# Kernel tuning notes

Measured on AMD Instinct MI355X. Metric: run time of the kernel, lower is better.

Reference implementation:

```python
import jax, jax.numpy as jnp
import numpy as np

KERNELS = (4, 4, 8, 8, 8, 16, 16)
HEADS = (4, 4, 8, 8, 8, 16, 16)
PATCH = 2
EPS = 1e-5


def _layer_norm(x, w, b):
    mu = jnp.mean(x, axis=-1, keepdims=True)
    var = jnp.mean(jnp.square(x - mu), axis=-1, keepdims=True)
    return (x - mu) * jax.lax.rsqrt(var + EPS) * w + b


def _sliding_kernel_attention(x, w_qkv, k, heads):
    # x: (B, H, W, C) channels-last. Unfold -> per-window attention over the
    # k*k pixels (token dim = C) -> overlap-add fold (stride 1).
    B, H, W, C = x.shape
    Lh, Lw = H - k + 1, W - k + 1
    scale = (C // heads) ** -0.5
    ih = jnp.arange(Lh)[:, None] + jnp.arange(k)[None, :]   # (Lh, k)
    iw = jnp.arange(Lw)[:, None] + jnp.arange(k)[None, :]   # (Lw, k)
    pat = x[:, ih][:, :, :, iw]                             # (B, Lh, k, Lw, k, C)
    tok = pat.transpose(0, 1, 3, 2, 4, 5).reshape(B, Lh * Lw, k * k, C)
    qkv = jnp.einsum('blnc,dc->blnd', tok, w_qkv)           # (B, L, k*k, 3C)
    q, kk, v = jnp.split(qkv, 3, axis=-1)
    attn = jax.nn.softmax(jnp.einsum('blqc,blkc->blqk', q, kk) * scale, axis=-1)
    o = jnp.einsum('blqk,blkc->blqc', attn, v)              # (B, L, k*k, C)
    o = o.reshape(B, Lh, Lw, k, k, C).transpose(0, 1, 3, 2, 4, 5)  # (B,Lh,k,Lw,k,C)
    # overlap-add fold back to (B, H, W, C); duplicate indices accumulate
    return jnp.zeros_like(x).at[:, ih[:, :, None, None], iw[None, None, :, :], :].add(o)


def _block(x, ln1_w, ln1_b, w_qkv, ln2_w, ln2_b, w1, b1, w2, b2, k, heads):
    x = x + _sliding_kernel_attention(_layer_norm(x, ln1_w, ln1_b), w_qkv, k, heads)
    h = _layer_norm(x, ln2_w, ln2_b)
    h = jax.nn.gelu(h @ w1.T + b1, approximate=False)
    return x + (h @ w2.T + b2)


def _forward(x, patch_w, patch_b, row_emb, col_emb, cls_tok, ln1_w, ln1_b, qkv_w,
             ln2_w, ln2_b, mlp_w1, mlp_b1, mlp_w2, mlp_b2, cls_w, cls_b):
    # patch embed: conv k=stride=PATCH; output laid out channels-last (B, G, G, C)
    h = jax.lax.conv_general_dilated(
        x, patch_w, (PATCH, PATCH), 'VALID',
        dimension_numbers=('NCHW', 'OIHW', 'NHWC')) + patch_b
    B, G, _, C = h.shape
    # 2D positional embedding: row half + col half concatenated on channels
    pos = jnp.concatenate([
        jnp.broadcast_to(row_emb[:, None, :], (G, G, C // 2)),
        jnp.broadcast_to(col_emb[None, :, :], (G, G, C // 2))], axis=-1)
    h = h + pos
    # cls token: one extra row prepended along H (torch cat on dim=2)
    cls = jnp.broadcast_to(cls_tok, (B, 1, G, C))
    h = jnp.concatenate([cls, h], axis=1)                   # (B, G+1, G, C)
    for i in range(7):
        h = _block(h, ln1_w[i], ln1_b[i], qkv_w[i], ln2_w[i], ln2_b[i],
                   mlp_w1[i], mlp_b1[i], mlp_w2[i], mlp_b2[i],
                   KERNELS[i], HEADS[i])
    return h[:, 0, 0, :] @ cls_w.T + cls_b                  # (B, num_classes)


def setup_inputs() -> dict:
    key = jax.random.key(0)
    ks = jax.random.split(key, 8)
    B, C, G, NCLS, NB = 16, 256, 16, 1000, 7
    s = 0.02
    return {
        'x': jax.random.normal(ks[0], (B, 3, 32, 32), jnp.float32),
        'patch_w': jax.random.normal(ks[1], (C, 3, PATCH, PATCH), jnp.float32) * s,
        'patch_b': jnp.zeros((C,), jnp.float32),
        'row_emb': jax.random.normal(ks[2], (G, C // 2), jnp.float32) * s,
        'col_emb': jax.random.normal(ks[3], (G, C // 2), jnp.float32) * s,
        'cls_tok': jnp.zeros((C,), jnp.float32),
        'ln1_w': jnp.ones((NB, C), jnp.float32),
        'ln1_b': jnp.zeros((NB, C), jnp.float32),
        'qkv_w': jax.random.normal(ks[4], (NB, 3 * C, C), jnp.float32) * s,
        'ln2_w': jnp.ones((NB, C), jnp.float32),
        'ln2_b': jnp.zeros((NB, C), jnp.float32),
        'mlp_w1': jax.random.normal(ks[5], (NB, 2 * C, C), jnp.float32) * s,
        'mlp_b1': jnp.zeros((NB, 2 * C), jnp.float32),
        'mlp_w2': jax.random.normal(ks[6], (NB, C, 2 * C), jnp.float32) * s,
        'mlp_b2': jnp.zeros((NB, C), jnp.float32),
        'cls_w': jax.random.normal(ks[7], (NCLS, C), jnp.float32) * s,
        'cls_b': jnp.zeros((NCLS,), jnp.float32),
    }


def reference(x, patch_w, patch_b, row_emb, col_emb, cls_tok, ln1_w, ln1_b, qkv_w,
              ln2_w, ln2_b, mlp_w1, mlp_b1, mlp_w2, mlp_b2, cls_w, cls_b):
    return _forward(x, patch_w, patch_b, row_emb, col_emb, cls_tok, ln1_w, ln1_b,
                    qkv_w, ln2_w, ln2_b, mlp_w1, mlp_b1, mlp_w2, mlp_b2, cls_w, cls_b)
```

## Files before the change

kernel.cpp:

```cpp
#include <hip/hip_runtime.h>
#include <cmath>

#define NPIX 4352
#define C_DIM 256

typedef unsigned short ushort_t;
typedef unsigned int uint_t;
typedef float f32x4 __attribute__((ext_vector_type(4)));
typedef __bf16 bfx8 __attribute__((ext_vector_type(8)));

__device__ __forceinline__ ushort_t f2bf(float f) {
    uint_t u = __float_as_uint(f);
    u = (u + 0x7FFFu + ((u >> 16) & 1u)) >> 16;
    return (ushort_t)u;
}
__device__ __forceinline__ float bf2f(ushort_t b) {
    return __uint_as_float(((uint_t)b) << 16);
}
__device__ __forceinline__ float gelu_f(float v) {
    return 0.5f * v * (1.0f + erff(v * 0.70710678118654752f));
}

__global__ __launch_bounds__(256) void conv3_bf16(
    const float* __restrict__ a, ushort_t* __restrict__ oa, int na,
    const float* __restrict__ b, ushort_t* __restrict__ ob, int nb,
    const float* __restrict__ c, ushort_t* __restrict__ oc, int nc)
{
    int ntot = na + nb + nc;
    for (int i = blockIdx.x * 256 + threadIdx.x; i < ntot; i += gridDim.x * 256) {
        if (i < na)            oa[i] = f2bf(a[i]);
        else if (i < na + nb)  ob[i - na] = f2bf(b[i - na]);
        else                   oc[i - na - nb] = f2bf(c[i - na - nb]);
    }
}

__global__ __launch_bounds__(256) void patch_embed_ln(
    const float* __restrict__ x, const float* __restrict__ pw,
    const float* __restrict__ pb, const float* __restrict__ row_emb,
    const float* __restrict__ col_emb, const float* __restrict__ cls_tok,
    const float* __restrict__ lw, const float* __restrict__ lb,
    float* __restrict__ out, ushort_t* __restrict__ lnout)
{
    __shared__ float red[8];
    int p = blockIdx.x;
    int c = threadIdx.x;
    int b = p / 272;
    int rem = p - b * 272;
    int y = rem >> 4;
    int xw = rem & 15;
    float v;
    if (y == 0) {
        v = cls_tok[c];
    } else {
        int gr = y - 1, gc = xw;
        const float* xb = x + (size_t)b * 3 * 1024;
        const float* wc = pw + (size_t)c * 12;
        float acc = pb[c];
        #pragma unroll
        for (int ci = 0; ci < 3; ci++)
            #pragma unroll
            for (int ph = 0; ph < 2; ph++)
                #pragma unroll
                for (int pq = 0; pq < 2; pq++)
                    acc += xb[ci * 1024 + (2 * gr + ph) * 32 + (2 * gc + pq)]
                         * wc[(ci * 2 + ph) * 2 + pq];
        acc += (c < 128) ? row_emb[gr * 128 + c] : col_emb[gc * 128 + (c - 128)];
        v = acc;
    }
    out[(size_t)p * C_DIM + c] = v;
    float s = v;
    s += __shfl_down(s, 32); s += __shfl_down(s, 16); s += __shfl_down(s, 8);
    s += __shfl_down(s, 4);  s += __shfl_down(s, 2);  s += __shfl_down(s, 1);
    if ((c & 63) == 0) red[c >> 6] = s;
    __syncthreads();
    float mu = (red[0] + red[1] + red[2] + red[3]) * (1.0f / 256.0f);
    float d = v - mu;
    float s2 = d * d;
    s2 += __shfl_down(s2, 32); s2 += __shfl_down(s2, 16); s2 += __shfl_down(s2, 8);
    s2 += __shfl_down(s2, 4);  s2 += __shfl_down(s2, 2);  s2 += __shfl_down(s2, 1);
    if ((c & 63) == 0) red[4 + (c >> 6)] = s2;
    __syncthreads();
    float var = (red[4] + red[5] + red[6] + red[7]) * (1.0f / 256.0f);
    lnout[(size_t)p * C_DIM + c] = f2bf(d * rsqrtf(var + 1e-5f) * lw[c] + lb[c]);
}

__global__ __launch_bounds__(256) void layernorm_k(
    const float* __restrict__ in, const float* __restrict__ w,
    const float* __restrict__ b, ushort_t* __restrict__ out)
{
    __shared__ float red[8];
    int r = blockIdx.x, c = threadIdx.x;
    float v = in[(size_t)r * C_DIM + c];
    float s = v;
    s += __shfl_down(s, 32); s += __shfl_down(s, 16); s += __shfl_down(s, 8);
    s += __shfl_down(s, 4);  s += __shfl_down(s, 2);  s += __shfl_down(s, 1);
    if ((c & 63) == 0) red[c >> 6] = s;
    __syncthreads();
    float mu = (red[0] + red[1] + red[2] + red[3]) * (1.0f / 256.0f);
    float d = v - mu;
    float s2 = d * d;
    s2 += __shfl_down(s2, 32); s2 += __shfl_down(s2, 16); s2 += __shfl_down(s2, 8);
    s2 += __shfl_down(s2, 4);  s2 += __shfl_down(s2, 2);  s2 += __shfl_down(s2, 1);
    if ((c & 63) == 0) red[4 + (c >> 6)] = s2;
    __syncthreads();
    float var = (red[4] + red[5] + red[6] + red[7]) * (1.0f / 256.0f);
    out[(size_t)r * C_DIM + c] = f2bf(d * rsqrtf(var + 1e-5f) * w[c] + b[c]);
}

template <int BM, int BN, int MODE>
__global__ __launch_bounds__(256) void gemm_v2(
    const ushort_t* __restrict__ A, const ushort_t* __restrict__ B,
    const float* __restrict__ bias, const float* __restrict__ res,
    void* __restrict__ outp, ushort_t* __restrict__ vT, int K, int ldo)
{
    constexpr int MI = BM / 32, NJ = BN / 32;
    constexpr int AG = BM * 4, BG = BN * 4;
    constexpr int AU = AG / 256, BU = BG / 256;
    constexpr int HALF = (BM + BN) * 32;
    constexpr int STAGE_E = 2 * HALF;
    constexpr int BOUNCE_E = BM * (BN + 8);
    constexpr int SMEM_E = (STAGE_E > BOUNCE_E) ? STAGE_E : BOUNCE_E;
    __shared__ ushort_t sm[SMEM_E];

    int m0 = blockIdx.x * BM, n0 = blockIdx.y * BN;
    int t = threadIdx.x, lane = t & 63, wv = t >> 6;
    int l15 = lane & 15, lg = lane >> 4;
    int wr = wv >> 1, wc = wv & 1;

    const int nt = K / 32;
    f32x4 acc[MI][NJ] = {};
    uint4 ra[AU], rb[BU];

    #pragma unroll
    for (int u = 0; u < AU; u++) {
        int g = t + u * 256, row = g >> 2, p = g & 3;
        int ps = p ^ ((row >> 1) & 3);
        ra[u] = *(const uint4*)(A + (size_t)(m0 + row) * K + ps * 8);
    }
    #pragma unroll
    for (int u = 0; u < BU; u++) {
        int g = t + u * 256, col = g >> 2, p = g & 3;
        int ps = p ^ ((col >> 1) & 3);
        rb[u] = *(const uint4*)(B + (size_t)(n0 + col) * K + ps * 8);
    }
    #pragma unroll
    for (int u = 0; u < AU; u++) *(uint4*)(sm + (t + u * 256) * 8) = ra[u];
    #pragma unroll
    for (int u = 0; u < BU; u++) *(uint4*)(sm + BM * 32 + (t + u * 256) * 8) = rb[u];
    __syncthreads();

    for (int ks = 0; ks < nt; ks++) {
        int coff = (ks & 1) * HALF, noff = ((ks & 1) ^ 1) * HALF;
        if (ks + 1 < nt) {
            int k1 = (ks + 1) * 32;
            #pragma unroll
            for (int u = 0; u < AU; u++) {
                int g = t + u * 256, row = g >> 2, p = g & 3;
                int ps = p ^ ((row >> 1) & 3);
                ra[u] = *(const uint4*)(A + (size_t)(m0 + row) * K + k1 + ps * 8);
            }
            #pragma unroll
            for (int u = 0; u < BU; u++) {
                int g = t + u * 256, col = g >> 2, p = g & 3;
                int ps = p ^ ((col >> 1) & 3);
                rb[u] = *(const uint4*)(B + (size_t)(n0 + col) * K + k1 + ps * 8);
            }
        }
        bfx8 af[MI], bf[NJ];
        #pragma unroll
        for (int i = 0; i < MI; i++) {
            int row = wr * (BM / 2) + i * 16 + l15;
            af[i] = *(const bfx8*)(sm + coff + row * 32 + ((lg ^ ((row >> 1) & 3)) << 3));
        }
        #pragma unroll
        for (int j = 0; j < NJ; j++) {
            int col = wc * (BN / 2) + j * 16 + l15;
            bf[j] = *(const bfx8*)(sm + coff + BM * 32 + col * 32 + ((lg ^ ((col >> 1) & 3)) << 3));
        }
        #pragma unroll
        for (int i = 0; i < MI; i++)
            #pragma unroll
            for (int j = 0; j < NJ; j++)
                acc[i][j] = __builtin_amdgcn_mfma_f32_16x16x32_bf16(af[i], bf[j], acc[i][j], 0, 0, 0);
        if (ks + 1 < nt) {
            #pragma unroll
            for (int u = 0; u < AU; u++) *(uint4*)(sm + noff + (t + u * 256) * 8) = ra[u];
            #pragma unroll
            for (int u = 0; u < BU; u++) *(uint4*)(sm + noff + BM * 32 + (t + u * 256) * 8) = rb[u];
        }
        __syncthreads();
    }

    if (MODE == 0 && n0 >= 512) {
        #pragma unroll
        for (int i = 0; i < MI; i++) {
            int mb = m0 + wr * (BM / 2) + i * 16 + lg * 4;
            #pragma unroll
            for (int j = 0; j < NJ; j++) {
                int nv = n0 - 512 + wc * (BN / 2) + j * 16 + l15;
                ushort4 pk;
                pk.x = f2bf(acc[i][j][0]); pk.y = f2bf(acc[i][j][1]);
                pk.z = f2bf(acc[i][j][2]); pk.w = f2bf(acc[i][j][3]);
                *(ushort4*)&vT[(size_t)nv * NPIX + mb] = pk;
            }
        }
        return;
    }
    if (MODE == 3) {
        float* o = (float*)outp;
        #pragma unroll
        for (int i = 0; i < MI; i++) {
            #pragma unroll
            for (int j = 0; j < NJ; j++) {
                int col = n0 + wc * (BN / 2) + j * 16 + l15;
                float bz = bias[col];
                #pragma unroll
                for (int r = 0; r < 4; r++) {
                    int row = m0 + wr * (BM / 2) + i * 16 + lg * 4 + r;
                    o[(size_t)row * ldo + col] = acc[i][j][r] + bz + res[(size_t)row * ldo + col];
                }
            }
        }
        return;
    }
    __syncthreads();
    #pragma unroll
    for (int i = 0; i < MI; i++) {
        #pragma unroll
        for (int j = 0; j < NJ; j++) {
            int cl = wc * (BN / 2) + j * 16 + l15;
            float bz = (MODE == 2) ? bias[n0 + cl] : 0.0f;
            #pragma unroll
            for (int r = 0; r < 4; r++) {
                int rl = wr * (BM / 2) + i * 16 + lg * 4 + r;
                float v = acc[i][j][r];
                if (MODE == 2) v = gelu_f(v + bz);
                sm[rl * (BN + 8) + cl] = f2bf(v);
            }
        }
    }
    __syncthreads();
    ushort_t* ob = (ushort_t*)outp;
    #pragma unroll
    for (int e = 0; e < BM * BN; e += 2048) {
        int idx = e + t * 8;
        int rl = idx / BN, cl = idx % BN;
        uint4 v = *(const uint4*)(sm + rl * (BN + 8) + cl);
        *(uint4*)&ob[(size_t)(m0 + rl) * ldo + n0 + cl] = v;
    }
}

__device__ __forceinline__ uint2 ld_u4_align(const uint_t* drow, int e0) {
    int d0 = e0 >> 1;
    if (!(e0 & 1)) return make_uint2(drow[d0], drow[d0 + 1]);
    uint_t a = drow[d0], b = drow[d0 + 1], c = drow[d0 + 2];
    return make_uint2((a >> 16) | (b << 16), (b >> 16) | (c << 16));
}
__device__ __forceinline__ uint4 ld_u8_align(const uint_t* drow, int e0) {
    int d0 = e0 >> 1;
    if (!(e0 & 1)) return make_uint4(drow[d0], drow[d0 + 1], drow[d0 + 2], drow[d0 + 3]);
    uint_t a = drow[d0], b = drow[d0 + 1], c = drow[d0 + 2], d = drow[d0 + 3], e = drow[d0 + 4];
    return make_uint4((a >> 16) | (b << 16), (b >> 16) | (c << 16),
                      (c >> 16) | (d << 16), (d >> 16) | (e << 16));
}

template <int KK>
__global__ __launch_bounds__(256) void attn_v2(
    const ushort_t* __restrict__ qk, const ushort_t* __restrict__ vT,
    ushort_t* __restrict__ obuf, int w0, int nW, float scale)
{
    constexpr int T = KK * KK;
    constexpr int Lh = 18 - KK, Lw = 17 - KK, L = Lh * Lw;
    constexpr int NF   = 1;
    constexpr int NJ   = 8;
    constexpr int PSTR = 40;
    constexpr int KROWS = 32;
    constexpr int VROWS = 256;
    constexpr int EOFF = 2048;
    constexpr int ESTR = 128;

    __shared__ ushort_t Klds[KROWS * 256];
    __shared__ ushort_t Vlds[VROWS * 64];
    __shared__ ushort_t Plds[4][16 * PSTR];

    int t = threadIdx.x, lane = t & 63, wv = t >> 6;
    int l15 = lane & 15, lg = lane >> 4;

    int wrel = blockIdx.x * 2 + (wv & 1);
    int wloc = wv & 1, chalf = wv >> 1, qbase = 0;
    if (wrel >= nW) wrel = nW - 1;

    int pbs[2];
    #pragma unroll
    for (int w = 0; w < 2; w++) {
        int wi = blockIdx.x * 2 + w;
        if (wi >= nW) wi = nW - 1;
        wi += w0;
        int b = wi / L, lrem = wi % L;
        pbs[w] = b * 272 + (lrem / Lw) * 16 + (lrem % Lw);
    }

    int qtok = qbase + l15;
    int qpix = pbs[wloc] + ((qtok >> 2) << 4) + (qtok & 3);
    bfx8 qf[8];
    #pragma unroll
    for (int cs = 0; cs < 8; cs++)
        qf[cs] = *(const bfx8*)(qk + (size_t)qpix * 512 + cs * 32 + lg * 8);

    f32x4 o[NJ] = {};
    float lsum[4] = {0.f, 0.f, 0.f, 0.f};

    for (int g = t; g < KROWS * 32; g += 256) {
        int row = g >> 5, cg = g & 31;
        int pix = pbs[row >> 4] + (((row & 15) >> 2) << 4) + (row & 3);
        uint4 v = *(const uint4*)(qk + (size_t)pix * 512 + 256 + cg * 8);
        *(uint4*)(Klds + row * 256 + ((cg ^ (row & 7)) << 3)) = v;
    }
    for (int g = t; g < VROWS * 8; g += 256) {
        int cr = g >> 3, c16 = g & 7;
        const uint_t* drow = (const uint_t*)(vT + (size_t)cr * NPIX);
        uint4 v;
        int w = c16 >> 2, sub = c16 & 3;
        if (sub < 2) {
            int pix0 = pbs[w] + (sub << 5);
            uint2 a  = ld_u4_align(drow, pix0);
            uint2 b2 = ld_u4_align(drow, pix0 + 16);
            v = make_uint4(a.x, a.y, b2.x, b2.y);
        } else v = make_uint4(0, 0, 0, 0);
        *(uint4*)(Vlds + cr * 64 + ((c16 ^ (cr & 7)) << 3)) = v;
    }
    __syncthreads();
    f32x4 s[NF];
    #pragma unroll
    for (int j = 0; j < NF; j++) s[j] = f32x4{0.f, 0.f, 0.f, 0.f};
    #pragma unroll
    for (int cs = 0; cs < 8; cs++) {
        int krow = (wloc << 4) + l15;
        bfx8 kf = *(const bfx8*)(Klds + krow * 256 + ((((cs << 2) + lg) ^ (krow & 7)) << 3));
        s[0] = __builtin_amdgcn_mfma_f32_16x16x32_bf16(qf[cs], kf, s[0], 0, 0, 0);
    }
    float p[NF][4];
    #pragma unroll
    for (int r = 0; r < 4; r++) {
        float mx = s[0][r];
        mx = fmaxf(mx, __shfl_xor(mx, 1));
        mx = fmaxf(mx, __shfl_xor(mx, 2));
        mx = fmaxf(mx, __shfl_xor(mx, 4));
        mx = fmaxf(mx, __shfl_xor(mx, 8));
        float ps = 0.f;
        p[0][r] = __expf(scale * (s[0][r] - mx));
        ps += p[0][r];
        ps += __shfl_xor(ps, 1);
        ps += __shfl_xor(ps, 2);
        ps += __shfl_xor(ps, 4);
        ps += __shfl_xor(ps, 8);
        lsum[r] = ps;
    }
    ushort_t* Pw = Plds[wv];
    #pragma unroll
    for (int r = 0; r < 4; r++) {
        Pw[(lg * 4 + r) * PSTR + l15] = f2bf(p[0][r]);
        Pw[(lg * 4 + r) * PSTR + 16 + l15] = 0;
    }
    asm volatile("s_waitcnt lgkmcnt(0)" ::: "memory");
    __builtin_amdgcn_sched_barrier(0);
    {
        bfx8 pf = *(const bfx8*)(Pw + l15 * PSTR + (lg << 3));
        #pragma unroll
        for (int j = 0; j < NJ; j++) {
            int cr = chalf * 128 + (j << 4) + l15;
            int c16 = ((wloc << 2) + lg) ^ (cr & 7);
            bfx8 vf = *(const bfx8*)(Vlds + cr * 64 + (c16 << 3));
            o[j] = __builtin_amdgcn_mfma_f32_16x16x32_bf16(pf, vf, o[j], 0, 0, 0);
        }
    }
    asm volatile("s_waitcnt lgkmcnt(0)" ::: "memory");
    __syncthreads();
    float inv[4];
    #pragma unroll
    for (int r = 0; r < 4; r++) inv[r] = 1.0f / lsum[r];
    ushort_t* Ep = Klds + wv * EOFF;
    #pragma unroll
    for (int j = 0; j < NJ; j++)
        #pragma unroll
        for (int r = 0; r < 4; r++)
            Ep[(lg * 4 + r) * ESTR + (j << 4) + l15] = f2bf(o[j][r] * inv[r]);
    asm volatile("s_waitcnt lgkmcnt(0)" ::: "memory");
    __builtin_amdgcn_sched_barrier(0);
    size_t gb = ((size_t)wrel * T + qbase) * C_DIM + chalf * 128;
    #pragma unroll
    for (int i = 0; i < 4; i++) {
        int off = i * 512 + lane * 8;
        int row = off >> 7, col = off & 127;
        uint4 v = *(const uint4*)(Ep + row * ESTR + col);
        *(uint4*)(obuf + gb + (size_t)row * C_DIM + col) = v;
    }
}

__global__ __launch_bounds__(256) void attn_v3(
    const ushort_t* __restrict__ qk, const ushort_t* __restrict__ vT,
    ushort_t* __restrict__ obuf, int w0, float scale)
{
    __shared__ ushort_t SH[32768];
    const int Lw = 9, L = 90;
    int t = threadIdx.x, lane = t & 63, wv = t >> 6;
    int l15 = lane & 15, lg = lane >> 4;
    int wrel = blockIdx.x;
    int widx = w0 + wrel;
    int b = widx / L, lrem = widx % L;
    int pbase = b * 272 + (lrem / Lw) * 16 + (lrem % Lw);
    int qbase = wv * 16;

    int qtok = qbase + l15;
    int qpix = pbase + ((qtok >> 3) << 4) + (qtok & 7);
    bfx8 qf[8];
    #pragma unroll
    for (int cs = 0; cs < 8; cs++)
        qf[cs] = *(const bfx8*)(qk + (size_t)qpix * 512 + cs * 32 + lg * 8);

    for (int g = t; g < 64 * 32; g += 256) {
        int row = g >> 5, cg = g & 31;
        int pix = pbase + ((row >> 3) << 4) + (row & 7);
        uint4 v = *(const uint4*)(qk + (size_t)pix * 512 + 256 + cg * 8);
        *(uint4*)(SH + row * 256 + ((cg ^ (row & 7)) << 3)) = v;
    }
    for (int g = t; g < 256 * 8; g += 256) {
        int cr = g >> 3, c16 = g & 7;
        const uint_t* drow = (const uint_t*)(vT + (size_t)cr * NPIX);
        uint4 v = ld_u8_align(drow, pbase + (c16 << 4));
        *(uint4*)(SH + 16384 + cr * 64 + ((c16 ^ (cr & 7)) << 3)) = v;
    }
    __syncthreads();

    f32x4 s[4];
    #pragma unroll
    for (int j = 0; j < 4; j++) s[j] = f32x4{0.f, 0.f, 0.f, 0.f};
    #pragma unroll
    for (int cs = 0; cs < 8; cs++) {
        #pragma unroll
        for (int j = 0; j < 4; j++) {
            int krow = (j << 4) + l15;
            bfx8 kf = *(const bfx8*)(SH + krow * 256 + ((((cs << 2) + lg) ^ (krow & 7)) << 3));
            s[j] = __builtin_amdgcn_mfma_f32_16x16x32_bf16(qf[cs], kf, s[j], 0, 0, 0);
        }
    }
    float p[4][4], lsum[4];
    #pragma unroll
    for (int r = 0; r < 4; r++) {
        float mx = s[0][r];
        #pragma unroll
        for (int j = 1; j < 4; j++) mx = fmaxf(mx, s[j][r]);
        mx = fmaxf(mx, __shfl_xor(mx, 1));
        mx = fmaxf(mx, __shfl_xor(mx, 2));
        mx = fmaxf(mx, __shfl_xor(mx, 4));
        mx = fmaxf(mx, __shfl_xor(mx, 8));
        float ps = 0.f;
        #pragma unroll
        for (int j = 0; j < 4; j++) {
            p[j][r] = __expf(scale * (s[j][r] - mx));
            ps += p[j][r];
        }
        ps += __shfl_xor(ps, 1);
        ps += __shfl_xor(ps, 2);
        ps += __shfl_xor(ps, 4);
        ps += __shfl_xor(ps, 8);
        lsum[r] = ps;
    }
    __syncthreads();
    ushort_t* Pw = SH + wv * 1088;
    #pragma unroll
    for (int j = 0; j < 4; j++)
        #pragma unroll
        for (int r = 0; r < 4; r++)
            Pw[(lg * 4 + r) * 68 + (j << 4) + l15] = f2bf(p[j][r]);
    asm volatile("s_waitcnt lgkmcnt(0)" ::: "memory");
    __builtin_amdgcn_sched_barrier(0);
    f32x4 o[16] = {};
    #pragma unroll
    for (int kt = 0; kt < 2; kt++) {
        bfx8 pf = *(const bfx8*)(Pw + l15 * 68 + (kt << 5) + (lg << 3));
        #pragma unroll
        for (int j = 0; j < 16; j++) {
            int cr = (j << 4) + l15;
            int c16 = ((kt << 2) + lg) ^ (cr & 7);
            bfx8 vf = *(const bfx8*)(SH + 16384 + cr * 64 + (c16 << 3));
            o[j] = __builtin_amdgcn_mfma_f32_16x16x32_bf16(pf, vf, o[j], 0, 0, 0);
        }
    }
    asm volatile("s_waitcnt lgkmcnt(0)" ::: "memory");
    __syncthreads();
    float inv[4];
    #pragma unroll
    for (int r = 0; r < 4; r++) inv[r] = 1.0f / lsum[r];
    ushort_t* Ep = SH + wv * 4224;
    #pragma unroll
    for (int j = 0; j < 16; j++)
        #pragma unroll
        for (int r = 0; r < 4; r++)
            Ep[(lg * 4 + r) * 260 + (j << 4) + l15] = f2bf(o[j][r] * inv[r]);
    asm volatile("s_waitcnt lgkmcnt(0)" ::: "memory");
    __builtin_amdgcn_sched_barrier(0);
    size_t gb = ((size_t)wrel * 64 + qbase) * C_DIM;
    #pragma unroll
    for (int i = 0; i < 8; i++) {
        int off = i * 512 + lane * 8;
        int row = off >> 8, col = off & 255;
        uint4 v = *(const uint4*)(Ep + row * 260 + col);
        *(uint4*)(obuf + gb + off) = v;
    }
}

template <int PASS>
__global__ __launch_bounds__(256) void gemm_seq(
    const ushort_t* __restrict__ A, const ushort_t* __restrict__ B,
    const float* __restrict__ linv, void* __restrict__ outp)
{
    __shared__ ushort_t sm[8192];
    int m0 = blockIdx.x * 64, n0 = blockIdx.y * 64;
    int seq = blockIdx.z;
    int pbase = (seq >> 1) * 272 + (seq & 1) * 16;
    int t = threadIdx.x, lane = t & 63, wv = t >> 6;
    int l15 = lane & 15, lg = lane >> 4;
    int wr = wv >> 1, wc = wv & 1;

    f32x4 acc[2][2] = {};
    uint4 ra, rb;

    int g_row = t >> 2, g_p = t & 3;
    int g_ps = g_p ^ ((g_row >> 1) & 3);

    const ushort_t* Asrc;
    const ushort_t* Bsrc;
    if (PASS == 0) {
        Asrc = A + (size_t)(pbase + m0 + g_row) * 512 + g_ps * 8;
        Bsrc = B + (size_t)(pbase + n0 + g_row) * 512 + 256 + g_ps * 8;
    } else {
        Asrc = A + (size_t)seq * 65536 + (size_t)(m0 + g_row) * 256 + g_ps * 8;
        Bsrc = B + (size_t)(n0 + g_row) * NPIX + pbase + g_ps * 8;
    }

    ra = *(const uint4*)(Asrc);
    rb = *(const uint4*)(Bsrc);
    *(uint4*)(sm + t * 8) = ra;
    *(uint4*)(sm + 2048 + t * 8) = rb;
    __syncthreads();

    for (int ks = 0; ks < 8; ks++) {
        int coff = (ks & 1) * 4096, noff = ((ks & 1) ^ 1) * 4096;
        if (ks + 1 < 8) {
            int k1 = (ks + 1) * 32;
            ra = *(const uint4*)(Asrc + k1);
            rb = *(const uint4*)(Bsrc + k1);
        }
        bfx8 af[2], bf[2];
        #pragma unroll
        for (int i = 0; i < 2; i++) {
            int row = wr * 32 + i * 16 + l15;
            af[i] = *(const bfx8*)(sm + coff + row * 32 + ((lg ^ ((row >> 1) & 3)) << 3));
        }
        #pragma unroll
        for (int j = 0; j < 2; j++) {
            int col = wc * 32 + j * 16 + l15;
            bf[j] = *(const bfx8*)(sm + coff + 2048 + col * 32 + ((lg ^ ((col >> 1) & 3)) << 3));
        }
        #pragma unroll
        for (int i = 0; i < 2; i++)
            #pragma unroll
            for (int j = 0; j < 2; j++)
                acc[i][j] = __builtin_amdgcn_mfma_f32_16x16x32_bf16(af[i], bf[j], acc[i][j], 0, 0, 0);
        if (ks + 1 < 8) {
            *(uint4*)(sm + noff + t * 8) = ra;
            *(uint4*)(sm + noff + 2048 + t * 8) = rb;
        }
        __syncthreads();
    }

    if (PASS == 0) {
        float* S = (float*)outp + (size_t)seq * 65536;
        #pragma unroll
        for (int i = 0; i < 2; i++) {
            #pragma unroll
            for (int j = 0; j < 2; j++) {
                int col = n0 + wc * 32 + j * 16 + l15;
                #pragma unroll
                for (int r = 0; r < 4; r++) {
                    int row = m0 + wr * 32 + i * 16 + lg * 4 + r;
                    S[(size_t)row * 256 + col] = acc[i][j][r];
                }
            }
        }
        return;
    }
    ushort_t* ob = (ushort_t*)outp;
    #pragma unroll
    for (int i = 0; i < 2; i++) {
        #pragma unroll
        for (int j = 0; j < 2; j++) {
            int cl = wc * 32 + j * 16 + l15;
            #pragma unroll
            for (int r = 0; r < 4; r++) {
                int rl = wr * 32 + i * 16 + lg * 4 + r;
                float v = acc[i][j][r] * linv[seq * 256 + m0 + rl];
                sm[rl * 72 + cl] = f2bf(v);
            }
        }
    }
    __syncthreads();
    #pragma unroll
    for (int e = 0; e < 4096; e += 2048) {
        int idx = e + t * 8;
        int rl = idx >> 6, cl = idx & 63;
        uint4 v = *(const uint4*)(sm + rl * 72 + cl);
        *(uint4*)&ob[(size_t)seq * 65536 + (size_t)(m0 + rl) * 256 + n0 + cl] = v;
    }
}

__global__ __launch_bounds__(256) void rowsm(
    const float* __restrict__ sbuf, ushort_t* __restrict__ pbuf,
    float* __restrict__ linv, float scale)
{
    __shared__ float red[8];
    int r = blockIdx.x, t = threadIdx.x;
    float s = sbuf[(size_t)r * 256 + t];
    float m = s;
    m = fmaxf(m, __shfl_down(m, 32)); m = fmaxf(m, __shfl_down(m, 16));
    m = fmaxf(m, __shfl_down(m, 8));  m = fmaxf(m, __shfl_down(m, 4));
    m = fmaxf(m, __shfl_down(m, 2));  m = fmaxf(m, __shfl_down(m, 1));
    if ((t & 63) == 0) red[t >> 6] = m;
    __syncthreads();
    m = fmaxf(fmaxf(red[0], red[1]), fmaxf(red[2], red[3]));
    float p = __expf(scale * (s - m));
    float ps = p;
    ps += __shfl_down(ps, 32); ps += __shfl_down(ps, 16); ps += __shfl_down(ps, 8);
    ps += __shfl_down(ps, 4);  ps += __shfl_down(ps, 2);  ps += __shfl_down(ps, 1);
    if ((t & 63) == 0) red[4 + (t >> 6)] = ps;
    __syncthreads();
    float sum = red[4] + red[5] + red[6] + red[7];
    pbuf[(size_t)r * 256 + t] = f2bf(p);
    if (t == 0) linv[r] = 1.0f / sum;
}

template <int K>
__global__ __launch_bounds__(256) void foldA(
    const ushort_t* __restrict__ obuf, float* __restrict__ rowsum)
{
    constexpr int Lh = 18 - K, Lw = 17 - K, L = Lh * Lw, T = K * K;
    int c = threadIdx.x;
    int bid = blockIdx.x;
    int dy = bid % K;
    int blh = bid / K;
    int lh = blh % Lh;
    int b = blh / Lh;
    float acc[16];
    #pragma unroll
    for (int x = 0; x < 16; x++) acc[x] = 0.f;
    const ushort_t* base = obuf + ((size_t)(b * L + lh * Lw) * T + dy * K) * C_DIM + c;
    #pragma unroll
    for (int lw = 0; lw < Lw; lw++)
        #pragma unroll
        for (int dx = 0; dx < K; dx++)
            acc[lw + dx] += bf2f(base[((size_t)lw * T + dx) * C_DIM]);
    float* orow = rowsum + (size_t)bid * 16 * C_DIM + c;
    #pragma unroll
    for (int x = 0; x < 16; x++) orow[(size_t)x * C_DIM] = acc[x];
}

template <int K>
__global__ __launch_bounds__(256) void foldB(
    const float* __restrict__ rowsum, const float* __restrict__ xin,
    float* __restrict__ y, const float* __restrict__ lw_,
    const float* __restrict__ lb_, ushort_t* __restrict__ lnout)
{
    constexpr int Lh = 18 - K;
    __shared__ float red[8];
    int p = blockIdx.x, c = threadIdx.x;
    int b = p / 272, rem = p - b * 272;
    int yy = rem >> 4, xx = rem & 15;
    float acc = xin[(size_t)p * C_DIM + c];
    #pragma unroll
    for (int dy = 0; dy < K; dy++) {
        int lh = yy - dy;
        if (lh >= 0 && lh < Lh)
            acc += rowsum[(((size_t)(b * Lh + lh) * K + dy) * 16 + xx) * C_DIM + c];
    }
    y[(size_t)p * C_DIM + c] = acc;
    float s = acc;
    s += __shfl_down(s, 32); s += __shfl_down(s, 16); s += __shfl_down(s, 8);
    s += __shfl_down(s, 4);  s += __shfl_down(s, 2);  s += __shfl_down(s, 1);
    if ((c & 63) == 0) red[c >> 6] = s;
    __syncthreads();
    float mu = (red[0] + red[1] + red[2] + red[3]) * (1.0f / 256.0f);
    float d = acc - mu;
    float s2 = d * d;
    s2 += __shfl_down(s2, 32); s2 += __shfl_down(s2, 16); s2 += __shfl_down(s2, 8);
    s2 += __shfl_down(s2, 4);  s2 += __shfl_down(s2, 2);  s2 += __shfl_down(s2, 1);
    if ((c & 63) == 0) red[4 + (c >> 6)] = s2;
    __syncthreads();
    float var = (red[4] + red[5] + red[6] + red[7]) * (1.0f / 256.0f);
    lnout[(size_t)p * C_DIM + c] = f2bf(d * rsqrtf(var + 1e-5f) * lw_[c] + lb_[c]);
}

__global__ __launch_bounds__(256) void fold_ln(
    const ushort_t* __restrict__ obuf, const float* __restrict__ xin,
    float* __restrict__ y, const float* __restrict__ lw,
    const float* __restrict__ lb, ushort_t* __restrict__ lnout, int do_ln,
    int k, int Lh, int Lw, int w0, int w1)
{
    __shared__ float red[8];
    int p = blockIdx.x;
    int c = threadIdx.x;
    int b = p / 272;
    int rem = p - b * 272;
    int yy = rem >> 4, xx = rem & 15;
    int L = Lh * Lw;
    int T = k * k;
    float acc = xin ? xin[(size_t)p * C_DIM + c] : y[(size_t)p * C_DIM + c];
    int lh0 = max(0, yy - k + 1), lh1 = min(Lh - 1, yy);
    int lw0 = max(0, xx - k + 1), lw1 = min(Lw - 1, xx);
    for (int lh = lh0; lh <= lh1; lh++) {
        for (int lw = lw0; lw <= lw1; lw++) {
            int widx = b * L + lh * Lw + lw;
            if (widx < w0 || widx >= w1) continue;
            int n = (yy - lh) * k + (xx - lw);
            acc += bf2f(obuf[((size_t)(widx - w0) * T + n) * C_DIM + c]);
        }
    }
    y[(size_t)p * C_DIM + c] = acc;
    if (!do_ln) return;
    float s = acc;
    s += __shfl_down(s, 32); s += __shfl_down(s, 16); s += __shfl_down(s, 8);
    s += __shfl_down(s, 4);  s += __shfl_down(s, 2);  s += __shfl_down(s, 1);
    if ((c & 63) == 0) red[c >> 6] = s;
    __syncthreads();
    float mu = (red[0] + red[1] + red[2] + red[3]) * (1.0f / 256.0f);
    float d = acc - mu;
    float s2 = d * d;
    s2 += __shfl_down(s2, 32); s2 += __shfl_down(s2, 16); s2 += __shfl_down(s2, 8);
    s2 += __shfl_down(s2, 4);  s2 += __shfl_down(s2, 2);  s2 += __shfl_down(s2, 1);
    if ((c & 63) == 0) red[4 + (c >> 6)] = s2;
    __syncthreads();
    float var = (red[4] + red[5] + red[6] + red[7]) * (1.0f / 256.0f);
    lnout[(size_t)p * C_DIM + c] = f2bf(d * rsqrtf(var + 1e-5f) * lw[c] + lb[c]);
}

__global__ __launch_bounds__(256) void classifier_k(
    const float* __restrict__ h, const float* __restrict__ cw,
    const float* __restrict__ cb, float* __restrict__ out)
{
    __shared__ float hrow[256];
    int b = blockIdx.x;
    int n = blockIdx.y * 256 + threadIdx.x;
    hrow[threadIdx.x] = h[(size_t)b * 272 * C_DIM + threadIdx.x];
    __syncthreads();
    if (n < 1000) {
        float acc = cb[n];
        const float* wr = cw + (size_t)n * C_DIM;
        for (int c = 0; c < 256; c++) acc += hrow[c] * wr[c];
        out[(size_t)b * 1000 + n] = acc;
    }
}

extern "C" void kernel_launch(void* const* d_in, const int* in_sizes, int n_in,
                              void* d_out, int out_size, void* d_ws, size_t ws_size,
                              hipStream_t stream)
{
    const float* x       = (const float*)d_in[0];
    const float* patch_w = (const float*)d_in[1];
    const float* patch_b = (const float*)d_in[2];
    const float* row_emb = (const float*)d_in[3];
    const float* col_emb = (const float*)d_in[4];
    const float* cls_tok = (const float*)d_in[5];
    const float* ln1_w   = (const float*)d_in[6];
    const float* ln1_b   = (const float*)d_in[7];
    const float* qkv_w   = (const float*)d_in[8];
    const float* ln2_w   = (const float*)d_in[9];
    const float* ln2_b   = (const float*)d_in[10];
    const float* mlp_w1  = (const float*)d_in[11];
    const float* mlp_b1  = (const float*)d_in[12];
    const float* mlp_w2  = (const float*)d_in[13];
    const float* mlp_b2  = (const float*)d_in[14];
    const float* cls_w   = (const float*)d_in[15];
    const float* cls_b   = (const float*)d_in[16];
    float* out = (float*)d_out;

    float* xb0  = (float*)d_ws;
    float* xb1  = xb0 + (size_t)NPIX * 256;
    ushort_t* lnb = (ushort_t*)(xb1 + (size_t)NPIX * 256);
    ushort_t* qkb = lnb + (size_t)NPIX * 256;
    ushort_t* vT  = qkb + (size_t)NPIX * 512;
    ushort_t* h1  = vT + (size_t)256 * NPIX;
    ushort_t* wq  = h1 + (size_t)NPIX * 512;
    ushort_t* w1b = wq + (size_t)7 * 768 * 256;
    ushort_t* w2b = w1b + (size_t)7 * 512 * 256;
    float* scratch = (float*)(w2b + (size_t)7 * 256 * 512);
    float* rowsum  = scratch;
    float* sbuf    = scratch;
    ushort_t* pbuf = (ushort_t*)(sbuf + (size_t)32 * 65536);
    float* linv    = (float*)(pbuf + (size_t)32 * 65536);
    ushort_t* obuf = (ushort_t*)(rowsum + 5242880);
    size_t obuf_off_bytes = (size_t)((char*)obuf - (char*)d_ws);
    size_t obuf_cap_e = (ws_size > obuf_off_bytes + 64)
                        ? (ws_size - obuf_off_bytes - 64) / 2 : 0;

    conv3_bf16<<<1024, 256, 0, stream>>>(qkv_w, wq, 7 * 768 * 256,
                                         mlp_w1, w1b, 7 * 512 * 256,
                                         mlp_w2, w2b, 7 * 256 * 512);

    patch_embed_ln<<<NPIX, 256, 0, stream>>>(x, patch_w, patch_b, row_emb,
                                             col_emb, cls_tok, ln1_w, ln1_b,
                                             xb0, lnb);

    const int KS[7] = {4, 4, 8, 8, 8, 16, 16};
    float* xcur = xb0;
    float* ybuf = xb1;

    for (int i = 0; i < 7; i++) {
        int k = KS[i];
        int Lh = 18 - k, Lw = 17 - k, L = Lh * Lw, T = k * k;
        float scale = 1.0f / std::sqrt((float)(256 / k));

        if (i > 0)
            layernorm_k<<<NPIX, 256, 0, stream>>>(xcur, ln1_w + i * 256,
                                                  ln1_b + i * 256, lnb);
        gemm_v2<128, 128, 0><<<dim3(NPIX / 128, 6), 256, 0, stream>>>(
            lnb, wq + (size_t)i * 768 * 256, nullptr, nullptr, qkb, vT, 256, 512);

        int totalW = 16 * L;
        if (k == 16) {
            gemm_seq<0><<<dim3(4, 4, 32), 256, 0, stream>>>(qkb, qkb, nullptr, sbuf);
            rowsm<<<8192, 256, 0, stream>>>(sbuf, pbuf, linv, scale);
            gemm_seq<1><<<dim3(4, 4, 32), 256, 0, stream>>>(pbuf, vT, linv, obuf);
            fold_ln<<<NPIX, 256, 0, stream>>>(obuf, xcur, ybuf,
                                              ln2_w + i * 256, ln2_b + i * 256,
                                              lnb, 1, k, Lh, Lw, 0, 32);
        } else if ((size_t)totalW * T * C_DIM <= obuf_cap_e) {
            if (k == 4) {
                attn_v2<4><<<(totalW + 1) / 2, 256, 0, stream>>>(qkb, vT, obuf, 0, totalW, scale);
                foldA<4><<<16 * 14 * 4, 256, 0, stream>>>(obuf, rowsum);
                foldB<4><<<NPIX, 256, 0, stream>>>(rowsum, xcur, ybuf,
                                                   ln2_w + i * 256, ln2_b + i * 256, lnb);
            } else {
                attn_v3<<<totalW, 256, 0, stream>>>(qkb, vT, obuf, 0, scale);
                foldA<8><<<16 * 10 * 8, 256, 0, stream>>>(obuf, rowsum);
                foldB<8><<<NPIX, 256, 0, stream>>>(rowsum, xcur, ybuf,
                                                   ln2_w + i * 256, ln2_b + i * 256, lnb);
            }
        } else {
            size_t perW = (size_t)T * C_DIM;
            int maxW = (int)(obuf_cap_e / perW);
            if (maxW < 2) maxW = 2;
            if (k == 4) maxW &= ~1;
            for (int w0 = 0; w0 < totalW; w0 += maxW) {
                int nW = totalW - w0 < maxW ? totalW - w0 : maxW;
                if (k == 4)
                    attn_v2<4><<<(nW + 1) / 2, 256, 0, stream>>>(qkb, vT, obuf, w0, nW, scale);
                else
                    attn_v3<<<nW, 256, 0, stream>>>(qkb, vT, obuf, w0, scale);
                int last = (w0 + nW >= totalW);
                fold_ln<<<NPIX, 256, 0, stream>>>(obuf, (w0 == 0) ? xcur : nullptr,
                                                  ybuf, ln2_w + i * 256, ln2_b + i * 256,
                                                  lnb, last, k, Lh, Lw, w0, w0 + nW);
            }
        }

        gemm_v2<64, 128, 2><<<dim3(NPIX / 64, 4), 256, 0, stream>>>(
            lnb, w1b + (size_t)i * 512 * 256, mlp_b1 + i * 512, nullptr, h1, nullptr, 256, 512);
        gemm_v2<64, 64, 3><<<dim3(NPIX / 64, 4), 256, 0, stream>>>(
            h1, w2b + (size_t)i * 256 * 512, mlp_b2 + i * 256, ybuf, xcur, nullptr, 512, 256);
    }

    classifier_k<<<dim3(16, 4), 256, 0, stream>>>(xcur, cls_w, cls_b, out);
}
```

Before: 644.2 us.

## Shrink attention LDS footprints and add specialized fold for k=16

The k=4 attention kernel is rewritten with a compact V layout (40-element padded rows holding only the two windows' 32 pixels instead of zero-padded 64), cutting shared memory. The k=8 kernel stages K in two 128-channel halves so its LDS drops from 64KB to 48KB, at the cost of an extra barrier and reload phase. A dedicated foldB16 kernel replaces the generic fold_ln for k=16, summing the two overlapping windows directly. The intent is higher occupancy and less fold overhead.

```diff
diff --git a/kernel.cpp b/kernel.cpp
--- a/kernel.cpp
+++ b/kernel.cpp
@@ -264,30 +264,16 @@
                       (c >> 16) | (d << 16), (d >> 16) | (e << 16));
 }
 
-template <int KK>
-__global__ __launch_bounds__(256) void attn_v2(
+__global__ __launch_bounds__(256) void attn_v4(
     const ushort_t* __restrict__ qk, const ushort_t* __restrict__ vT,
     ushort_t* __restrict__ obuf, int w0, int nW, float scale)
 {
-    constexpr int T = KK * KK;
-    constexpr int Lh = 18 - KK, Lw = 17 - KK, L = Lh * Lw;
-    constexpr int NF   = 1;
-    constexpr int NJ   = 8;
-    constexpr int PSTR = 40;
-    constexpr int KROWS = 32;
-    constexpr int VROWS = 256;
-    constexpr int EOFF = 2048;
-    constexpr int ESTR = 128;
-
-    __shared__ ushort_t Klds[KROWS * 256];
-    __shared__ ushort_t Vlds[VROWS * 64];
-    __shared__ ushort_t Plds[4][16 * PSTR];
-
+    __shared__ ushort_t SH[20992];
+    const int Lw = 13, L = 182;
     int t = threadIdx.x, lane = t & 63, wv = t >> 6;
     int l15 = lane & 15, lg = lane >> 4;
-
-    int wrel = blockIdx.x * 2 + (wv & 1);
-    int wloc = wv & 1, chalf = wv >> 1, qbase = 0;
+    int wloc = wv & 1, chalf = wv >> 1;
+    int wrel = blockIdx.x * 2 + wloc;
     if (wrel >= nW) wrel = nW - 1;
 
     int pbs[2];
@@ -300,77 +286,68 @@
         pbs[w] = b * 272 + (lrem / Lw) * 16 + (lrem % Lw);
     }
 
-    int qtok = qbase + l15;
-    int qpix = pbs[wloc] + ((qtok >> 2) << 4) + (qtok & 3);
+    int qpix = pbs[wloc] + ((l15 >> 2) << 4) + (l15 & 3);
     bfx8 qf[8];
     #pragma unroll
     for (int cs = 0; cs < 8; cs++)
         qf[cs] = *(const bfx8*)(qk + (size_t)qpix * 512 + cs * 32 + lg * 8);
 
-    f32x4 o[NJ] = {};
-    float lsum[4] = {0.f, 0.f, 0.f, 0.f};
-
-    for (int g = t; g < KROWS * 32; g += 256) {
+    for (int g = t; g < 32 * 32; g += 256) {
         int row = g >> 5, cg = g & 31;
         int pix = pbs[row >> 4] + (((row & 15) >> 2) << 4) + (row & 3);
         uint4 v = *(const uint4*)(qk + (size_t)pix * 512 + 256 + cg * 8);
-        *(uint4*)(Klds + row * 256 + ((cg ^ (row & 7)) << 3)) = v;
-    }
-    for (int g = t; g < VROWS * 8; g += 256) {
-        int cr = g >> 3, c16 = g & 7;
+        *(uint4*)(SH + row * 256 + ((cg ^ (row & 7)) << 3)) = v;
+    }
+    for (int g = t; g < 256 * 4; g += 256) {
+        int cr = g >> 2, q8 = g & 3;
+        int w = q8 >> 1, sub = q8 & 1;
         const uint_t* drow = (const uint_t*)(vT + (size_t)cr * NPIX);
-        uint4 v;
-        int w = c16 >> 2, sub = c16 & 3;
-        if (sub < 2) {
-            int pix0 = pbs[w] + (sub << 5);
-            uint2 a  = ld_u4_align(drow, pix0);
-            uint2 b2 = ld_u4_align(drow, pix0 + 16);
-            v = make_uint4(a.x, a.y, b2.x, b2.y);
-        } else v = make_uint4(0, 0, 0, 0);
-        *(uint4*)(Vlds + cr * 64 + ((c16 ^ (cr & 7)) << 3)) = v;
-    }
-    __syncthreads();
-    f32x4 s[NF];
-    #pragma unroll
-    for (int j = 0; j < NF; j++) s[j] = f32x4{0.f, 0.f, 0.f, 0.f};
+        int pix0 = pbs[w] + (sub << 5);
+        uint2 a  = ld_u4_align(drow, pix0);
+        uint2 b2 = ld_u4_align(drow, pix0 + 16);
+        uint4 v = make_uint4(a.x, a.y, b2.x, b2.y);
+        *(uint4*)(SH + 8192 + cr * 40 + q8 * 8) = v;
+    }
+    __syncthreads();
+
+    f32x4 s0 = {};
     #pragma unroll
     for (int cs = 0; cs < 8; cs++) {
         int krow = (wloc << 4) + l15;
-        bfx8 kf = *(const bfx8*)(Klds + krow * 256 + ((((cs << 2) + lg) ^ (krow & 7)) << 3));
-        s[0] = __builtin_amdgcn_mfma_f32_16x16x32_bf16(qf[cs], kf, s[0], 0, 0, 0);
-    }
-    float p[NF][4];
+        bfx8 kf = *(const bfx8*)(SH + krow * 256 + ((((cs << 2) + lg) ^ (krow & 7)) << 3));
+        s0 = __builtin_amdgcn_mfma_f32_16x16x32_bf16(qf[cs], kf, s0, 0, 0, 0);
+    }
+    float p4[4], lsum[4];
     #pragma unroll
     for (int r = 0; r < 4; r++) {
-        float mx = s[0][r];
+        float mx = s0[r];
         mx = fmaxf(mx, __shfl_xor(mx, 1));
         mx = fmaxf(mx, __shfl_xor(mx, 2));
         mx = fmaxf(mx, __shfl_xor(mx, 4));
         mx = fmaxf(mx, __shfl_xor(mx, 8));
-        float ps = 0.f;
-        p[0][r] = __expf(scale * (s[0][r] - mx));
-        ps += p[0][r];
+        p4[r] = __expf(scale * (s0[r] - mx));
+        float ps = p4[r];
         ps += __shfl_xor(ps, 1);
         ps += __shfl_xor(ps, 2);
         ps += __shfl_xor(ps, 4);
         ps += __shfl_xor(ps, 8);
         lsum[r] = ps;
     }
-    ushort_t* Pw = Plds[wv];
+    ushort_t* Pw = SH + 18432 + wv * 640;
     #pragma unroll
     for (int r = 0; r < 4; r++) {
-        Pw[(lg * 4 + r) * PSTR + l15] = f2bf(p[0][r]);
-        Pw[(lg * 4 + r) * PSTR + 16 + l15] = 0;
+        Pw[(lg * 4 + r) * 40 + (wloc << 4) + l15] = f2bf(p4[r]);
+        Pw[(lg * 4 + r) * 40 + ((wloc ^ 1) << 4) + l15] = 0;
     }
     asm volatile("s_waitcnt lgkmcnt(0)" ::: "memory");
     __builtin_amdgcn_sched_barrier(0);
+    f32x4 o[8] = {};
     {
-        bfx8 pf = *(const bfx8*)(Pw + l15 * PSTR + (lg << 3));
-        #pragma unroll
-        for (int j = 0; j < NJ; j++) {
-            int cr = chalf * 128 + (j << 4) + l15;
-            int c16 = ((wloc << 2) + lg) ^ (cr & 7);
-            bfx8 vf = *(const bfx8*)(Vlds + cr * 64 + (c16 << 3));
+        bfx8 pf = *(const bfx8*)(Pw + l15 * 40 + (lg << 3));
+        #pragma unroll
+        for (int j = 0; j < 8; j++) {
+            int c = chalf * 128 + (j << 4) + l15;
+            bfx8 vf = *(const bfx8*)(SH + 8192 + c * 40 + (lg << 3));
             o[j] = __builtin_amdgcn_mfma_f32_16x16x32_bf16(pf, vf, o[j], 0, 0, 0);
         }
     }
@@ -379,20 +356,20 @@
     float inv[4];
     #pragma unroll
     for (int r = 0; r < 4; r++) inv[r] = 1.0f / lsum[r];
-    ushort_t* Ep = Klds + wv * EOFF;
-    #pragma unroll
-    for (int j = 0; j < NJ; j++)
+    ushort_t* Ep = SH + wv * 2176;
+    #pragma unroll
+    for (int j = 0; j < 8; j++)
         #pragma unroll
         for (int r = 0; r < 4; r++)
-            Ep[(lg * 4 + r) * ESTR + (j << 4) + l15] = f2bf(o[j][r] * inv[r]);
+            Ep[(lg * 4 + r) * 136 + (j << 4) + l15] = f2bf(o[j][r] * inv[r]);
     asm volatile("s_waitcnt lgkmcnt(0)" ::: "memory");
     __builtin_amdgcn_sched_barrier(0);
-    size_t gb = ((size_t)wrel * T + qbase) * C_DIM + chalf * 128;
+    size_t gb = ((size_t)wrel * 16) * C_DIM + chalf * 128;
     #pragma unroll
     for (int i = 0; i < 4; i++) {
         int off = i * 512 + lane * 8;
         int row = off >> 7, col = off & 127;
-        uint4 v = *(const uint4*)(Ep + row * ESTR + col);
+        uint4 v = *(const uint4*)(Ep + row * 136 + col);
         *(uint4*)(obuf + gb + (size_t)row * C_DIM + col) = v;
     }
 }
@@ -401,7 +378,7 @@
     const ushort_t* __restrict__ qk, const ushort_t* __restrict__ vT,
     ushort_t* __restrict__ obuf, int w0, float scale)
 {
-    __shared__ ushort_t SH[32768];
+    __shared__ ushort_t SH[24576];
     const int Lw = 9, L = 90;
     int t = threadIdx.x, lane = t & 63, wv = t >> 6;
     int l15 = lane & 15, lg = lane >> 4;
@@ -418,17 +395,17 @@
     for (int cs = 0; cs < 8; cs++)
         qf[cs] = *(const bfx8*)(qk + (size_t)qpix * 512 + cs * 32 + lg * 8);
 
-    for (int g = t; g < 64 * 32; g += 256) {
-        int row = g >> 5, cg = g & 31;
+    for (int g = t; g < 64 * 16; g += 256) {
+        int row = g >> 4, cg = g & 15;
         int pix = pbase + ((row >> 3) << 4) + (row & 7);
         uint4 v = *(const uint4*)(qk + (size_t)pix * 512 + 256 + cg * 8);
-        *(uint4*)(SH + row * 256 + ((cg ^ (row & 7)) << 3)) = v;
+        *(uint4*)(SH + row * 128 + ((cg ^ (row & 7)) << 3)) = v;
     }
     for (int g = t; g < 256 * 8; g += 256) {
         int cr = g >> 3, c16 = g & 7;
         const uint_t* drow = (const uint_t*)(vT + (size_t)cr * NPIX);
         uint4 v = ld_u8_align(drow, pbase + (c16 << 4));
-        *(uint4*)(SH + 16384 + cr * 64 + ((c16 ^ (cr & 7)) << 3)) = v;
+        *(uint4*)(SH + 8192 + cr * 64 + ((c16 ^ (cr & 7)) << 3)) = v;
     }
     __syncthreads();
 
@@ -436,11 +413,28 @@
     #pragma unroll
     for (int j = 0; j < 4; j++) s[j] = f32x4{0.f, 0.f, 0.f, 0.f};
     #pragma unroll
-    for (int cs = 0; cs < 8; cs++) {
+    for (int cs = 0; cs < 4; cs++) {
         #pragma unroll
         for (int j = 0; j < 4; j++) {
             int krow = (j << 4) + l15;
-            bfx8 kf = *(const bfx8*)(SH + krow * 256 + ((((cs << 2) + lg) ^ (krow & 7)) << 3));
+            bfx8 kf = *(const bfx8*)(SH + krow * 128 + ((((cs << 2) + lg) ^ (krow & 7)) << 3));
+            s[j] = __builtin_amdgcn_mfma_f32_16x16x32_bf16(qf[cs], kf, s[j], 0, 0, 0);
+        }
+    }
+    __syncthreads();
+    for (int g = t; g < 64 * 16; g += 256) {
+        int row = g >> 4, cg = g & 15;
+        int pix = pbase + ((row >> 3) << 4) + (row & 7);
+        uint4 v = *(const uint4*)(qk + (size_t)pix * 512 + 384 + cg * 8);
+        *(uint4*)(SH + row * 128 + ((cg ^ (row & 7)) << 3)) = v;
+    }
+    __syncthreads();
+    #pragma unroll
+    for (int cs = 4; cs < 8; cs++) {
+        #pragma unroll
+        for (int j = 0; j < 4; j++) {
+            int krow = (j << 4) + l15;
+            bfx8 kf = *(const bfx8*)(SH + krow * 128 + (((((cs - 4) << 2) + lg) ^ (krow & 7)) << 3));
             s[j] = __builtin_amdgcn_mfma_f32_16x16x32_bf16(qf[cs], kf, s[j], 0, 0, 0);
         }
     }
@@ -483,7 +477,7 @@
         for (int j = 0; j < 16; j++) {
             int cr = (j << 4) + l15;
             int c16 = ((kt << 2) + lg) ^ (cr & 7);
-            bfx8 vf = *(const bfx8*)(SH + 16384 + cr * 64 + (c16 << 3));
+            bfx8 vf = *(const bfx8*)(SH + 8192 + cr * 64 + (c16 << 3));
             o[j] = __builtin_amdgcn_mfma_f32_16x16x32_bf16(pf, vf, o[j], 0, 0, 0);
         }
     }
@@ -497,7 +491,7 @@
     for (int j = 0; j < 16; j++)
         #pragma unroll
         for (int r = 0; r < 4; r++)
-            Ep[(lg * 4 + r) * 260 + (j << 4) + l15] = f2bf(o[j][r] * inv[r]);
+            Ep[(lg * 4 + r) * 264 + (j << 4) + l15] = f2bf(o[j][r] * inv[r]);
     asm volatile("s_waitcnt lgkmcnt(0)" ::: "memory");
     __builtin_amdgcn_sched_barrier(0);
     size_t gb = ((size_t)wrel * 64 + qbase) * C_DIM;
@@ -505,7 +499,7 @@
     for (int i = 0; i < 8; i++) {
         int off = i * 512 + lane * 8;
         int row = off >> 8, col = off & 255;
-        uint4 v = *(const uint4*)(Ep + row * 260 + col);
+        uint4 v = *(const uint4*)(Ep + row * 264 + col);
         *(uint4*)(obuf + gb + off) = v;
     }
 }
@@ -683,6 +677,37 @@
         if (lh >= 0 && lh < Lh)
             acc += rowsum[(((size_t)(b * Lh + lh) * K + dy) * 16 + xx) * C_DIM + c];
     }
+    y[(size_t)p * C_DIM + c] = acc;
+    float s = acc;
+    s += __shfl_down(s, 32); s += __shfl_down(s, 16); s += __shfl_down(s, 8);
+    s += __shfl_down(s, 4);  s += __shfl_down(s, 2);  s += __shfl_down(s, 1);
+    if ((c & 63) == 0) red[c >> 6] = s;
+    __syncthreads();
+    float mu = (red[0] + red[1] + red[2] + red[3]) * (1.0f / 256.0f);
+    float d = acc - mu;
+    float s2 = d * d;
+    s2 += __shfl_down(s2, 32); s2 += __shfl_down(s2, 16); s2 += __shfl_down(s2, 8);
+    s2 += __shfl_down(s2, 4);  s2 += __shfl_down(s2, 2);  s2 += __shfl_down(s2, 1);
+    if ((c & 63) == 0) red[4 + (c >> 6)] = s2;
+    __syncthreads();
+    float var = (red[4] + red[5] + red[6] + red[7]) * (1.0f / 256.0f);
+    lnout[(size_t)p * C_DIM + c] = f2bf(d * rsqrtf(var + 1e-5f) * lw_[c] + lb_[c]);
+}
+
+__global__ __launch_bounds__(256) void foldB16(
+    const ushort_t* __restrict__ obuf, const float* __restrict__ xin,
+    float* __restrict__ y, const float* __restrict__ lw_,
+    const float* __restrict__ lb_, ushort_t* __restrict__ lnout)
+{
+    __shared__ float red[8];
+    int p = blockIdx.x, c = threadIdx.x;
+    int b = p / 272, rem = p - b * 272;
+    int yy = rem >> 4, xx = rem & 15;
+    float acc = xin[(size_t)p * C_DIM + c];
+    if (yy <= 15)
+        acc += bf2f(obuf[((size_t)(b * 2) * 256 + (yy * 16 + xx)) * C_DIM + c]);
+    if (yy >= 1)
+        acc += bf2f(obuf[((size_t)(b * 2 + 1) * 256 + ((yy - 1) * 16 + xx)) * C_DIM + c]);
     y[(size_t)p * C_DIM + c] = acc;
     float s = acc;
     s += __shfl_down(s, 32); s += __shfl_down(s, 16); s += __shfl_down(s, 8);
@@ -830,12 +855,11 @@
             gemm_seq<0><<<dim3(4, 4, 32), 256, 0, stream>>>(qkb, qkb, nullptr, sbuf);
             rowsm<<<8192, 256, 0, stream>>>(sbuf, pbuf, linv, scale);
             gemm_seq<1><<<dim3(4, 4, 32), 256, 0, stream>>>(pbuf, vT, linv, obuf);
-            fold_ln<<<NPIX, 256, 0, stream>>>(obuf, xcur, ybuf,
-                                              ln2_w + i * 256, ln2_b + i * 256,
-                                              lnb, 1, k, Lh, Lw, 0, 32);
+            foldB16<<<NPIX, 256, 0, stream>>>(obuf, xcur, ybuf,
+                                              ln2_w + i * 256, ln2_b + i * 256, lnb);
         } else if ((size_t)totalW * T * C_DIM <= obuf_cap_e) {
             if (k == 4) {
-                attn_v2<4><<<(totalW + 1) / 2, 256, 0, stream>>>(qkb, vT, obuf, 0, totalW, scale);
+                attn_v4<<<(totalW + 1) / 2, 256, 0, stream>>>(qkb, vT, obuf, 0, totalW, scale);
                 foldA<4><<<16 * 14 * 4, 256, 0, stream>>>(obuf, rowsum);
                 foldB<4><<<NPIX, 256, 0, stream>>>(rowsum, xcur, ybuf,
                                                    ln2_w + i * 256, ln2_b + i * 256, lnb);
@@ -853,7 +877,7 @@
             for (int w0 = 0; w0 < totalW; w0 += maxW) {
                 int nW = totalW - w0 < maxW ? totalW - w0 : maxW;
                 if (k == 4)
-                    attn_v2<4><<<(nW + 1) / 2, 256, 0, stream>>>(qkb, vT, obuf, w0, nW, scale);
+                    attn_v4<<<(nW + 1) / 2, 256, 0, stream>>>(qkb, vT, obuf, w0, nW, scale);
                 else
                     attn_v3<<<nW, 256, 0, stream>>>(qkb, vT, obuf, w0, scale);
                 int last = (w0 + nW >= totalW);
```

Result: no change. 633.4 us (-1.7%).
